# Optimization experiments

Measured on AMD Instinct MI355X. Metric: run time of the kernel, lower is better.

Reference implementation:

```python
import jax, jax.numpy as jnp
from jax import lax
import numpy as np

EPS = 1e-08
BETA_VAL = 0.9
B_VAL = 1.0
SIGMA_VAL = 10.0

@jax.custom_vjp
def spike_fn(mthr, sigma):
    # Heaviside forward; SuperSpike surrogate gradient in backward
    return (mthr > 0).astype(mthr.dtype)

def _spike_fwd(mthr, sigma):
    return (mthr > 0).astype(mthr.dtype), (mthr, sigma)

def _spike_bwd(res, g):
    mthr, sigma = res
    grad = g / (sigma * jnp.abs(mthr) + 1.0) ** 2
    return grad, jnp.zeros_like(sigma)

spike_fn.defvjp(_spike_fwd, _spike_bwd)


def setup_inputs() -> dict:
    key = jax.random.key(0)
    kx, kw, kv = jax.random.split(key, 3)
    B, T, I, O = 128, 100, 1024, 1024
    x = jax.random.normal(kx, (B, T, I), dtype=jnp.float32)
    w = (jax.random.normal(kw, (I, O), dtype=jnp.float32)
         * np.float32(np.sqrt(1.0 / I)))  # mean 0, std w_init_std*sqrt(1/I)
    v = (jax.random.normal(kv, (O, O), dtype=jnp.float32)
         * np.float32(np.sqrt(1.0 / O)))
    beta = jnp.full((1,), BETA_VAL, dtype=jnp.float32)   # one_per_layer
    b = jnp.full((O,), B_VAL, dtype=jnp.float32)
    sigma = jnp.full((O,), SIGMA_VAL, dtype=jnp.float32)  # surrogate_sigma_mode='all'
    return {"x": x, "w": w, "v": v, "beta": beta, "b": b, "sigma": sigma}


def reference(x, w, v, beta, b, sigma):
    B, T, I = x.shape
    O = w.shape[1]
    h = jnp.einsum('bti,io->bto', x, w)            # [B,T,O]
    d = jnp.einsum('ai,ao->io', w, w)              # lateral term w^T w, [O,O]
    norm = (w ** 2).sum(0)                         # [O]
    inv_norm = 1.0 / (norm + EPS)

    mem0 = jnp.zeros((B, O), dtype=x.dtype)
    spk0 = jnp.zeros((B, O), dtype=x.dtype)

    def step(carry, h_t):
        mem, spk = carry
        rst = spk @ d                              # lateral reset [B,O]
        inp = h_t + spk @ v                        # recurrent input
        # Leaky neuron, soft reset
        mem = (mem - rst) * beta + inp * (1.0 - beta)
        mthr = mem * inv_norm - b
        spk = spike_fn(mthr, sigma)
        return (mem, spk), spk

    h_t_first = jnp.swapaxes(h, 0, 1)              # [T,B,O]
    _, spk_seq = lax.scan(step, (mem0, spk0), h_t_first)
    spk_rec = jnp.swapaxes(spk_seq, 0, 1)          # [B,T,O]

    loss = 0.5 * (spk_rec ** 2).mean()             # Regularization 'squared'
    spk_spread_loss = spk_rec.sum(axis=(0, 2)).max() / (B * O)  # 'max'
    return spk_rec, loss, spk_spread_loss
```

## Files before the change

### kernel.cpp

```cpp
#include <hip/hip_runtime.h>
#include <cstdint>
#include <cstddef>

#define I_DIM 1024
#define O_DIM 1024
#define B_DIM 128
#define T_DIM 100
#define PANEL 32768
#define QSTep 512

typedef __attribute__((ext_vector_type(8))) __bf16 bf16x8;
typedef __attribute__((ext_vector_type(16))) float f32x16;

__device__ __forceinline__ void wg_barrier_lgkm() {
  __asm__ volatile("" ::: "memory");
  __builtin_amdgcn_s_waitcnt(0xC07F);
  __builtin_amdgcn_s_barrier();
  __asm__ volatile("" ::: "memory");
}

__device__ __forceinline__ unsigned short bf16rn(float x) {
  unsigned u = __float_as_uint(x);
  unsigned r = u + 0x7FFFu + ((u >> 16) & 1u);
  return (unsigned short)(r >> 16);
}
__device__ __forceinline__ void split2(float x, unsigned short& h,
                                       unsigned short& l) {
  h = bf16rn(x);
  float hf = __uint_as_float(((unsigned)h) << 16);
  l = bf16rn(x - hf);
}

__global__ __launch_bounds__(256) void prep_kernel(
    const float* __restrict__ w, const float* __restrict__ x,
    unsigned short* __restrict__ wTth, unsigned short* __restrict__ wTtl,
    unsigned short* __restrict__ xth, unsigned short* __restrict__ xtl,
    double* __restrict__ normpart) {
  __shared__ float tile[64][65];
  __shared__ double red[4][64];
  const int id = blockIdx.x;
  const int tid = threadIdx.x;
  if (id < 256) {
    const int a0 = (id >> 4) * 64, o0 = (id & 15) * 64;
    const int tr = tid >> 4, tc4 = (tid & 15) * 4;
#pragma unroll
    for (int rr = 0; rr < 64; rr += 16) {
      float4 v = *(const float4*)&w[(size_t)(a0 + tr + rr) * O_DIM + o0 + tc4];
      tile[tr + rr][tc4 + 0] = v.x;
      tile[tr + rr][tc4 + 1] = v.y;
      tile[tr + rr][tc4 + 2] = v.z;
      tile[tr + rr][tc4 + 3] = v.w;
    }
    __syncthreads();
    {
      const int ol = tid & 63, seg = tid >> 6;
      double s = 0.0;
#pragma unroll
      for (int i = 0; i < 16; ++i) {
        double v = (double)tile[seg * 16 + i][ol];
        s += v * v;
      }
      red[seg][ol] = s;
    }
    const int q = (a0 >> 4) + (tc4 >> 4);
    const int kh = (tc4 >> 3) & 1;
    const int inner = tc4 & 7;
#pragma unroll
    for (int rr = 0; rr < 64; rr += 16) {
      int o = o0 + tr + rr;
      unsigned short hh[4], ll[4];
#pragma unroll
      for (int j = 0; j < 4; ++j) split2(tile[tc4 + j][tr + rr], hh[j], ll[j]);
      int l = (o & 31) + 32 * kh;
      size_t base = ((size_t)(o >> 5) * PANEL) + (size_t)q * QSTep +
                    (size_t)l * 8 + inner;
      *(ushort4*)&wTth[base] = make_ushort4(hh[0], hh[1], hh[2], hh[3]);
      *(ushort4*)&wTtl[base] = make_ushort4(ll[0], ll[1], ll[2], ll[3]);
    }
    __syncthreads();
    if (tid < 64)
      normpart[(size_t)(a0 >> 6) * O_DIM + o0 + tid] =
          red[0][tid] + red[1][tid] + red[2][tid] + red[3][tid];
  } else {
    const int p = (id - 256) >> 2, sub = (id - 256) & 3;
    const int wq = tid >> 6, lane = tid & 63;
    const int row = lane & 31, kh = lane >> 5;
    const float* src = x + (size_t)(p * 32 + row) * I_DIM + kh * 8;
#pragma unroll
    for (int i = sub * 4; i < sub * 4 + 4; ++i) {
      const int q = i * 4 + wq;
      const float* s = src + q * 16;
      float4 v0 = *(const float4*)(s);
      float4 v1 = *(const float4*)(s + 4);
      unsigned short h[8], l[8];
      split2(v0.x, h[0], l[0]);
      split2(v0.y, h[1], l[1]);
      split2(v0.z, h[2], l[2]);
      split2(v0.w, h[3], l[3]);
      split2(v1.x, h[4], l[4]);
      split2(v1.y, h[5], l[5]);
      split2(v1.z, h[6], l[6]);
      split2(v1.w, h[7], l[7]);
      size_t base = ((size_t)p * PANEL) + (size_t)q * QSTep + (size_t)lane * 8;
      *(ushort4*)&xth[base] = make_ushort4(h[0], h[1], h[2], h[3]);
      *(ushort4*)&xth[base + 4] = make_ushort4(h[4], h[5], h[6], h[7]);
      *(ushort4*)&xtl[base] = make_ushort4(l[0], l[1], l[2], l[3]);
      *(ushort4*)&xtl[base + 4] = make_ushort4(l[4], l[5], l[6], l[7]);
    }
  }
}

__global__ __launch_bounds__(256, 3) void gemm_fused(
    const unsigned short* __restrict__ xth,
    const unsigned short* __restrict__ xtl,
    const unsigned short* __restrict__ wTth,
    const unsigned short* __restrict__ wTtl, const float* __restrict__ v,
    const float* __restrict__ beta_p, float* __restrict__ h,
    float* __restrict__ M) {
  const int tid = threadIdx.x;
  const int wv = tid >> 6, lane = tid & 63;
  const int lm = lane & 31, lkh = lane >> 5;
  if (blockIdx.y < 100) {
    const int row0 = blockIdx.y * 128, col0 = blockIdx.x * 64;
    const int wm = wv >> 1, wn = wv & 1;
    f32x16 acc[2];
#pragma unroll
    for (int a = 0; a < 2; ++a)
#pragma unroll
      for (int e = 0; e < 16; ++e) acc[a][e] = 0.f;
    const unsigned short *pah[2], *pal[2], *pbh, *pbl;
#pragma unroll
    for (int mt = 0; mt < 2; ++mt) {
      size_t offA =
          ((size_t)((row0 >> 5) + wm * 2 + mt) * PANEL) + (size_t)lane * 8;
      pah[mt] = xth + offA;
      pal[mt] = xtl + offA;
    }
    {
      size_t offB = ((size_t)((col0 >> 5) + wn) * PANEL) + (size_t)lane * 8;
      pbh = wTth + offB;
      pbl = wTtl + offB;
    }
    bf16x8 fah[2][2][2], fal[2][2][2], fbh[2][2], fbl[2][2];
#pragma unroll
    for (int qq = 0; qq < 2; ++qq) {
      size_t d = (size_t)qq * QSTep;
#pragma unroll
      for (int mt = 0; mt < 2; ++mt) {
        fah[0][qq][mt] = *(const bf16x8*)(pah[mt] + d);
        fal[0][qq][mt] = *(const bf16x8*)(pal[mt] + d);
      }
      fbh[0][qq] = *(const bf16x8*)(pbh + d);
      fbl[0][qq] = *(const bf16x8*)(pbl + d);
    }
#pragma unroll 2
    for (int qp = 0; qp < 32; ++qp) {
      const int cb = qp & 1;
      if (qp < 31) {
        size_t dp = (size_t)(qp + 1) * (2 * QSTep);
#pragma unroll
        for (int qq = 0; qq < 2; ++qq) {
          size_t d = dp + (size_t)qq * QSTep;
#pragma unroll
          for (int mt = 0; mt < 2; ++mt) {
            fah[cb ^ 1][qq][mt] = *(const bf16x8*)(pah[mt] + d);
            fal[cb ^ 1][qq][mt] = *(const bf16x8*)(pal[mt] + d);
          }
          fbh[cb ^ 1][qq] = *(const bf16x8*)(pbh + d);
          fbl[cb ^ 1][qq] = *(const bf16x8*)(pbl + d);
        }
      }
#pragma unroll
      for (int qq = 0; qq < 2; ++qq) {
#pragma unroll
        for (int mt = 0; mt < 2; ++mt)
          acc[mt] = __builtin_amdgcn_mfma_f32_32x32x16_bf16(
              fah[cb][qq][mt], fbh[cb][qq], acc[mt], 0, 0, 0);
#pragma unroll
        for (int mt = 0; mt < 2; ++mt)
          acc[mt] = __builtin_amdgcn_mfma_f32_32x32x16_bf16(
              fah[cb][qq][mt], fbl[cb][qq], acc[mt], 0, 0, 0);
#pragma unroll
        for (int mt = 0; mt < 2; ++mt)
          acc[mt] = __builtin_amdgcn_mfma_f32_32x32x16_bf16(
              fal[cb][qq][mt], fbh[cb][qq], acc[mt], 0, 0, 0);
      }
    }
    const int col = col0 + wn * 32 + lm;
#pragma unroll
    for (int mt = 0; mt < 2; ++mt)
#pragma unroll
      for (int r = 0; r < 16; ++r) {
        int row = row0 + wm * 64 + mt * 32 + (r & 3) + 8 * (r >> 2) + 4 * lkh;
        h[(size_t)row * O_DIM + col] = acc[mt][r];
      }
  } else {
    const int i0 = (blockIdx.y - 100) * 64, o0 = blockIdx.x * 64;
    const int wm = wv >> 1, wn = wv & 1;
    f32x16 acc;
#pragma unroll
    for (int e = 0; e < 16; ++e) acc[e] = 0.f;
    const size_t offA = ((size_t)((i0 >> 5) + wm) * PANEL) + (size_t)lane * 8;
    const size_t offB = ((size_t)((o0 >> 5) + wn) * PANEL) + (size_t)lane * 8;
    bf16x8 ah[2], al[2], bh[2], bl[2];
    ah[0] = *(const bf16x8*)(wTth + offA);
    al[0] = *(const bf16x8*)(wTtl + offA);
    bh[0] = *(const bf16x8*)(wTth + offB);
    bl[0] = *(const bf16x8*)(wTtl + offB);
#pragma unroll 2
    for (int q = 0; q < 64; ++q) {
      const int cb = q & 1;
      if (q < 63) {
        size_t d = (size_t)(q + 1) * QSTep;
        ah[cb ^ 1] = *(const bf16x8*)(wTth + offA + d);
        al[cb ^ 1] = *(const bf16x8*)(wTtl + offA + d);
        bh[cb ^ 1] = *(const bf16x8*)(wTth + offB + d);
        bl[cb ^ 1] = *(const bf16x8*)(wTtl + offB + d);
      }
      acc =
          __builtin_amdgcn_mfma_f32_32x32x16_bf16(ah[cb], bh[cb], acc, 0, 0, 0);
      acc =
          __builtin_amdgcn_mfma_f32_32x32x16_bf16(ah[cb], bl[cb], acc, 0, 0, 0);
      acc =
          __builtin_amdgcn_mfma_f32_32x32x16_bf16(al[cb], bh[cb], acc, 0, 0, 0);
    }
    const float beta = beta_p[0];
    const float ombeta = 1.0f - beta;
    const int col = o0 + wn * 32 + lm;
#pragma unroll
    for (int r = 0; r < 16; ++r) {
      int row = i0 + wm * 32 + (r & 3) + 8 * (r >> 2) + 4 * lkh;
      M[(size_t)row * O_DIM + col] =
          ombeta * v[(size_t)row * O_DIM + col] - beta * acc[r];
    }
  }
}

__global__ __launch_bounds__(256) void scan_kernel(
    const float* __restrict__ h, const float* __restrict__ M,
    const double* __restrict__ normpart, const float* __restrict__ bvec,
    const float* __restrict__ beta_p, float* __restrict__ out,
    int* __restrict__ wgcnt, int* __restrict__ done) {
  __shared__ unsigned short wlist[2][4][256];
  __shared__ int wcnt[2][4];
  __shared__ int reds[128];
  __shared__ int lastflag;
  const int b = blockIdx.x, tid = threadIdx.x;
  const int wv = tid >> 6;
  const int ob4 = tid * 4;
  const double beta = (double)beta_p[0];
  const double ombeta = 1.0 - beta;
  double mem[4] = {0.0, 0.0, 0.0, 0.0};
  double inv[4], bth[4];
#pragma unroll
  for (int j = 0; j < 4; ++j) {
    double s = 0.0;
#pragma unroll
    for (int g = 0; g < 16; ++g) s += normpart[(size_t)g * O_DIM + ob4 + j];
    inv[j] = 1.0 / (s + 1e-8);
    bth[j] = (double)bvec[ob4 + j];
  }
  if (tid < 8) wcnt[tid >> 2][tid & 3] = 0;
  __syncthreads();
  const float* hb = h + (size_t)b * T_DIM * O_DIM;
  float* obp = out + (size_t)b * T_DIM * O_DIM;
  float4 hv0 = *(const float4*)&hb[ob4];
  float4 hv1 = *(const float4*)&hb[O_DIM + ob4];
  for (int t = 0; t < T_DIM; ++t) {
    const int p = t & 1, np = p ^ 1;
    float4 hv2 = make_float4(0.f, 0.f, 0.f, 0.f);
    if (t + 2 < T_DIM) hv2 = *(const float4*)&hb[(size_t)(t + 2) * O_DIM + ob4];
    double lat[4] = {0.0, 0.0, 0.0, 0.0};
    const int ks = wcnt[p][0] + wcnt[p][1] + wcnt[p][2] + wcnt[p][3];
    if (ks) {
#pragma unroll
      for (int w = 0; w < 4; ++w) {
        const int kw = wcnt[p][w];
        for (int n = 0; n < kw; ++n) {
          const int i = wlist[p][w][n];
          float4 m = *(const float4*)&M[(size_t)i * O_DIM + ob4];
          lat[0] += (double)m.x;
          lat[1] += (double)m.y;
          lat[2] += (double)m.z;
          lat[3] += (double)m.w;
        }
      }
    }
    const float hvv[4] = {hv0.x, hv0.y, hv0.z, hv0.w};
    float os[4];
    unsigned cur = 0;
#pragma unroll
    for (int j = 0; j < 4; ++j) {
      mem[j] = mem[j] * beta + (double)hvv[j] * ombeta + lat[j];
      double mthr = mem[j] * inv[j] - bth[j];
      bool s = mthr > 0.0;
      os[j] = s ? 1.0f : 0.0f;
      unsigned long long mask = __ballot(s);
      if (s) {
        unsigned below = __builtin_amdgcn_mbcnt_lo((unsigned)mask, 0);
        below = __builtin_amdgcn_mbcnt_hi((unsigned)(mask >> 32), below);
        wlist[np][wv][cur + below] = (unsigned short)(ob4 + j);
      }
      cur += (unsigned)__popcll(mask);
    }
    *(float4*)&obp[(size_t)t * O_DIM + ob4] =
        make_float4(os[0], os[1], os[2], os[3]);
    hv0 = hv1;
    hv1 = hv2;
    if ((tid & 63) == 0) wcnt[np][wv] = (int)cur;
    wg_barrier_lgkm();
    if (tid == 0)
      wgcnt[b * T_DIM + t] =
          wcnt[np][0] + wcnt[np][1] + wcnt[np][2] + wcnt[np][3];
  }
  __threadfence();
  if (tid == 0) {
    int old = atomicAdd(done, 1);
    lastflag = (old == B_DIM - 1) ? 1 : 0;
  }
  __syncthreads();
  if (lastflag) {
    __threadfence();
    int s = 0;
    if (tid < T_DIM) {
      for (int bb = 0; bb < B_DIM; ++bb) s += wgcnt[bb * T_DIM + tid];
    }
    if (tid < 128) reds[tid] = (tid < T_DIM) ? s : 0;
    __syncthreads();
    if (tid == 0) {
      long long total = 0;
      int mx = 0;
      for (int i = 0; i < T_DIM; ++i) {
        total += reds[i];
        if (reds[i] > mx) mx = reds[i];
      }
      const double N = (double)B_DIM * T_DIM * O_DIM;
      out[(size_t)B_DIM * T_DIM * O_DIM] = (float)(0.5 * (double)total / N);
      out[(size_t)B_DIM * T_DIM * O_DIM + 1] =
          (float)((double)mx / (double)(B_DIM * O_DIM));
    }
  }
}

extern "C" void kernel_launch(void* const* d_in, const int* in_sizes, int n_in,
                              void* d_out, int out_size, void* d_ws,
                              size_t ws_size, hipStream_t stream) {
  const float* x = (const float*)d_in[0];
  const float* w = (const float*)d_in[1];
  const float* v = (const float*)d_in[2];
  const float* beta = (const float*)d_in[3];
  const float* b = (const float*)d_in[4];
  float* out = (float*)d_out;

  char* ws = (char*)d_ws;
  const size_t OFF_M = 0;
  const size_t OFF_H = 4194304;
  const size_t OFF_WTH = 56623104;
  const size_t OFF_WTL = 58720256;
  const size_t OFF_NP = 60817408;
  const size_t OFF_DONE = 60948480;
  const size_t OFF_XTH = 60948992;
  const size_t OFF_XTL = 87163392;
  float* M = (float*)(ws + OFF_M);
  float* h = (float*)(ws + OFF_H);
  unsigned short* wTth = (unsigned short*)(ws + OFF_WTH);
  unsigned short* wTtl = (unsigned short*)(ws + OFF_WTL);
  double* normpart = (double*)(ws + OFF_NP);
  int* done = (int*)(ws + OFF_DONE);
  unsigned short* xth = (unsigned short*)(ws + OFF_XTH);
  unsigned short* xtl = (unsigned short*)(ws + OFF_XTL);
  int* wgcnt = (int*)(ws + OFF_XTH);

  hipMemsetAsync(done, 0, 512, stream);
  hipLaunchKernelGGL(prep_kernel, dim3(1856), dim3(256), 0, stream, w, x, wTth,
                     wTtl, xth, xtl, normpart);
  hipLaunchKernelGGL(gemm_fused, dim3(16, 116), dim3(256), 0, stream, xth, xtl,
                     wTth, wTtl, v, beta, h, M);
  hipLaunchKernelGGL(scan_kernel, dim3(128), dim3(256), 0, stream, h, M,
                     normpart, b, beta, out, wgcnt, done);
}
```

Measured before the change: 321.5 us.

## Enlarge fused GEMM tiles to 128x128 with 8 waves and unify both branches

The fused GEMM kernel now uses 512-thread blocks with 8 waves, each computing a 128x128 output tile. Both the h=x·w branch and the w^T w branch share one code path with a single-step K loop. The grid shrinks from 16x116 to 8x108 blocks. The aim is more operand reuse per block from the larger tiles and a uniform tile shape for the lateral-matrix GEMM. The trade-off is fewer blocks, a shallower prefetch per iteration, and occupancy that now depends on the new launch bounds.

```diff
diff --git a/kernel.cpp b/kernel.cpp
--- a/kernel.cpp
+++ b/kernel.cpp
@@ -110,7 +110,7 @@
   }
 }
 
-__global__ __launch_bounds__(256, 3) void gemm_fused(
+__global__ __launch_bounds__(512, 5) void gemm_fused(
     const unsigned short* __restrict__ xth,
     const unsigned short* __restrict__ xtl,
     const unsigned short* __restrict__ wTth,
@@ -119,120 +119,87 @@
     float* __restrict__ M) {
   const int tid = threadIdx.x;
   const int wv = tid >> 6, lane = tid & 63;
+  const int wm = wv >> 2, wn = wv & 3;
   const int lm = lane & 31, lkh = lane >> 5;
-  if (blockIdx.y < 100) {
-    const int row0 = blockIdx.y * 128, col0 = blockIdx.x * 64;
-    const int wm = wv >> 1, wn = wv & 1;
-    f32x16 acc[2];
-#pragma unroll
-    for (int a = 0; a < 2; ++a)
-#pragma unroll
-      for (int e = 0; e < 16; ++e) acc[a][e] = 0.f;
-    const unsigned short *pah[2], *pal[2], *pbh, *pbl;
-#pragma unroll
-    for (int mt = 0; mt < 2; ++mt) {
-      size_t offA =
-          ((size_t)((row0 >> 5) + wm * 2 + mt) * PANEL) + (size_t)lane * 8;
-      pah[mt] = xth + offA;
-      pal[mt] = xtl + offA;
-    }
-    {
-      size_t offB = ((size_t)((col0 >> 5) + wn) * PANEL) + (size_t)lane * 8;
-      pbh = wTth + offB;
-      pbl = wTtl + offB;
-    }
-    bf16x8 fah[2][2][2], fal[2][2][2], fbh[2][2], fbl[2][2];
-#pragma unroll
-    for (int qq = 0; qq < 2; ++qq) {
-      size_t d = (size_t)qq * QSTep;
+  const bool is_h = blockIdx.y < 100;
+  const int rbase = is_h ? (int)blockIdx.y * 128 : ((int)blockIdx.y - 100) * 128;
+  const int cbase = (int)blockIdx.x * 128;
+  const unsigned short* Ah_src = is_h ? xth : wTth;
+  const unsigned short* Al_src = is_h ? xtl : wTtl;
+
+  f32x16 acc[2];
+#pragma unroll
+  for (int a = 0; a < 2; ++a)
+#pragma unroll
+    for (int e = 0; e < 16; ++e) acc[a][e] = 0.f;
+
+  const unsigned short *pah[2], *pal[2], *pbh, *pbl;
+#pragma unroll
+  for (int mt = 0; mt < 2; ++mt) {
+    size_t offA =
+        ((size_t)((rbase >> 5) + wm * 2 + mt) * PANEL) + (size_t)lane * 8;
+    pah[mt] = Ah_src + offA;
+    pal[mt] = Al_src + offA;
+  }
+  {
+    size_t offB = ((size_t)((cbase >> 5) + wn) * PANEL) + (size_t)lane * 8;
+    pbh = wTth + offB;
+    pbl = wTtl + offB;
+  }
+  bf16x8 fah[2][2], fal[2][2], fbh[2], fbl[2];
+#pragma unroll
+  for (int mt = 0; mt < 2; ++mt) {
+    fah[0][mt] = *(const bf16x8*)(pah[mt]);
+    fal[0][mt] = *(const bf16x8*)(pal[mt]);
+  }
+  fbh[0] = *(const bf16x8*)(pbh);
+  fbl[0] = *(const bf16x8*)(pbl);
+#pragma unroll 2
+  for (int q = 0; q < 64; ++q) {
+    const int cb = q & 1;
+    if (q < 63) {
+      size_t d = (size_t)(q + 1) * QSTep;
 #pragma unroll
       for (int mt = 0; mt < 2; ++mt) {
-        fah[0][qq][mt] = *(const bf16x8*)(pah[mt] + d);
-        fal[0][qq][mt] = *(const bf16x8*)(pal[mt] + d);
-      }
-      fbh[0][qq] = *(const bf16x8*)(pbh + d);
-      fbl[0][qq] = *(const bf16x8*)(pbl + d);
-    }
-#pragma unroll 2
-    for (int qp = 0; qp < 32; ++qp) {
-      const int cb = qp & 1;
-      if (qp < 31) {
-        size_t dp = (size_t)(qp + 1) * (2 * QSTep);
-#pragma unroll
-        for (int qq = 0; qq < 2; ++qq) {
-          size_t d = dp + (size_t)qq * QSTep;
-#pragma unroll
-          for (int mt = 0; mt < 2; ++mt) {
-            fah[cb ^ 1][qq][mt] = *(const bf16x8*)(pah[mt] + d);
-            fal[cb ^ 1][qq][mt] = *(const bf16x8*)(pal[mt] + d);
-          }
-          fbh[cb ^ 1][qq] = *(const bf16x8*)(pbh + d);
-          fbl[cb ^ 1][qq] = *(const bf16x8*)(pbl + d);
-        }
-      }
-#pragma unroll
-      for (int qq = 0; qq < 2; ++qq) {
-#pragma unroll
-        for (int mt = 0; mt < 2; ++mt)
-          acc[mt] = __builtin_amdgcn_mfma_f32_32x32x16_bf16(
-              fah[cb][qq][mt], fbh[cb][qq], acc[mt], 0, 0, 0);
-#pragma unroll
-        for (int mt = 0; mt < 2; ++mt)
-          acc[mt] = __builtin_amdgcn_mfma_f32_32x32x16_bf16(
-              fah[cb][qq][mt], fbl[cb][qq], acc[mt], 0, 0, 0);
-#pragma unroll
-        for (int mt = 0; mt < 2; ++mt)
-          acc[mt] = __builtin_amdgcn_mfma_f32_32x32x16_bf16(
-              fal[cb][qq][mt], fbh[cb][qq], acc[mt], 0, 0, 0);
-      }
-    }
-    const int col = col0 + wn * 32 + lm;
+        fah[cb ^ 1][mt] = *(const bf16x8*)(pah[mt] + d);
+        fal[cb ^ 1][mt] = *(const bf16x8*)(pal[mt] + d);
+      }
+      fbh[cb ^ 1] = *(const bf16x8*)(pbh + d);
+      fbl[cb ^ 1] = *(const bf16x8*)(pbl + d);
+    }
+#pragma unroll
+    for (int mt = 0; mt < 2; ++mt)
+      acc[mt] = __builtin_amdgcn_mfma_f32_32x32x16_bf16(fah[cb][mt], fbh[cb],
+                                                        acc[mt], 0, 0, 0);
+#pragma unroll
+    for (int mt = 0; mt < 2; ++mt)
+      acc[mt] = __builtin_amdgcn_mfma_f32_32x32x16_bf16(fah[cb][mt], fbl[cb],
+                                                        acc[mt], 0, 0, 0);
+#pragma unroll
+    for (int mt = 0; mt < 2; ++mt)
+      acc[mt] = __builtin_amdgcn_mfma_f32_32x32x16_bf16(fal[cb][mt], fbh[cb],
+                                                        acc[mt], 0, 0, 0);
+  }
+  const int col = cbase + wn * 32 + lm;
+  if (is_h) {
 #pragma unroll
     for (int mt = 0; mt < 2; ++mt)
 #pragma unroll
       for (int r = 0; r < 16; ++r) {
-        int row = row0 + wm * 64 + mt * 32 + (r & 3) + 8 * (r >> 2) + 4 * lkh;
+        int row = rbase + wm * 64 + mt * 32 + (r & 3) + 8 * (r >> 2) + 4 * lkh;
         h[(size_t)row * O_DIM + col] = acc[mt][r];
       }
   } else {
-    const int i0 = (blockIdx.y - 100) * 64, o0 = blockIdx.x * 64;
-    const int wm = wv >> 1, wn = wv & 1;
-    f32x16 acc;
-#pragma unroll
-    for (int e = 0; e < 16; ++e) acc[e] = 0.f;
-    const size_t offA = ((size_t)((i0 >> 5) + wm) * PANEL) + (size_t)lane * 8;
-    const size_t offB = ((size_t)((o0 >> 5) + wn) * PANEL) + (size_t)lane * 8;
-    bf16x8 ah[2], al[2], bh[2], bl[2];
-    ah[0] = *(const bf16x8*)(wTth + offA);
-    al[0] = *(const bf16x8*)(wTtl + offA);
-    bh[0] = *(const bf16x8*)(wTth + offB);
-    bl[0] = *(const bf16x8*)(wTtl + offB);
-#pragma unroll 2
-    for (int q = 0; q < 64; ++q) {
-      const int cb = q & 1;
-      if (q < 63) {
-        size_t d = (size_t)(q + 1) * QSTep;
-        ah[cb ^ 1] = *(const bf16x8*)(wTth + offA + d);
-        al[cb ^ 1] = *(const bf16x8*)(wTtl + offA + d);
-        bh[cb ^ 1] = *(const bf16x8*)(wTth + offB + d);
-        bl[cb ^ 1] = *(const bf16x8*)(wTtl + offB + d);
-      }
-      acc =
-          __builtin_amdgcn_mfma_f32_32x32x16_bf16(ah[cb], bh[cb], acc, 0, 0, 0);
-      acc =
-          __builtin_amdgcn_mfma_f32_32x32x16_bf16(ah[cb], bl[cb], acc, 0, 0, 0);
-      acc =
-          __builtin_amdgcn_mfma_f32_32x32x16_bf16(al[cb], bh[cb], acc, 0, 0, 0);
-    }
     const float beta = beta_p[0];
     const float ombeta = 1.0f - beta;
-    const int col = o0 + wn * 32 + lm;
-#pragma unroll
-    for (int r = 0; r < 16; ++r) {
-      int row = i0 + wm * 32 + (r & 3) + 8 * (r >> 2) + 4 * lkh;
-      M[(size_t)row * O_DIM + col] =
-          ombeta * v[(size_t)row * O_DIM + col] - beta * acc[r];
-    }
+#pragma unroll
+    for (int mt = 0; mt < 2; ++mt)
+#pragma unroll
+      for (int r = 0; r < 16; ++r) {
+        int row = rbase + wm * 64 + mt * 32 + (r & 3) + 8 * (r >> 2) + 4 * lkh;
+        M[(size_t)row * O_DIM + col] =
+            ombeta * v[(size_t)row * O_DIM + col] - beta * acc[mt][r];
+      }
   }
 }
 
@@ -374,7 +341,7 @@
   hipMemsetAsync(done, 0, 512, stream);
   hipLaunchKernelGGL(prep_kernel, dim3(1856), dim3(256), 0, stream, w, x, wTth,
                      wTtl, xth, xtl, normpart);
-  hipLaunchKernelGGL(gemm_fused, dim3(16, 116), dim3(256), 0, stream, xth, xtl,
+  hipLaunchKernelGGL(gemm_fused, dim3(8, 108), dim3(512), 0, stream, xth, xtl,
                      wTth, wTtl, v, beta, h, M);
   hipLaunchKernelGGL(scan_kernel, dim3(128), dim3(256), 0, stream, h, M,
                      normpart, b, beta, out, wgcnt, done);
```

Measured after the change: 331.6 us. 1.03x slower.
